# Kernel tuning notes

Measured on AMD Instinct MI355X. Metric: run time of the kernel, lower is better.

Reference implementation:

```python
import jax, jax.numpy as jnp
import numpy as np

B, E, C, M, H = 4, 8, 512, 1024, 4096

def setup_inputs() -> dict:
    key = jax.random.key(0)
    k1, k2, k3, k4, k5 = jax.random.split(key, 5)
    s = 1.0 / np.sqrt(M)
    return {
        "x": jax.random.normal(k1, (B, E, C, M), dtype=jnp.float32),
        "fc1_weight": jax.random.normal(k2, (E, H, M), dtype=jnp.float32) * s,
        "fc1_bias": jax.random.normal(k3, (E, 1, H), dtype=jnp.float32) * 0.02,
        "fc2_weight": jax.random.normal(k4, (E, H, M), dtype=jnp.float32) * (1.0 / np.sqrt(H)),
        "fc2_bias": jax.random.normal(k5, (E, 1, M), dtype=jnp.float32) * 0.02,
    }

def reference(x, fc1_weight, fc1_bias, fc2_weight, fc2_bias):
    # x: [B, E, C, M] -> [E, B*C, M]
    b, e, c, m = x.shape
    xe = jnp.transpose(x, (1, 0, 2, 3)).reshape(e, b * c, m)
    # fc1: [E,T,M] @ [E,M,H] (fp32 grouped GEMM with bias)
    h = jnp.einsum('etm,ehm->eth', xe.astype(jnp.float32), fc1_weight.astype(jnp.float32)) + fc1_bias.astype(jnp.float32)
    h = jax.nn.relu(h)
    # fc2: [E,T,H] @ [E,H,M] + bias (dropout is identity)
    o = jnp.einsum('eth,ehm->etm', h, fc2_weight) + fc2_bias
    o = o.reshape(e, b, c, m)
    return jnp.transpose(o, (1, 0, 2, 3))
```

## Files before the change

### kernel.cpp

```cpp
#include <hip/hip_runtime.h>
#include <hip/hip_bf16.h>

typedef __bf16 bf16x8 __attribute__((ext_vector_type(8)));
typedef float  f32x4  __attribute__((ext_vector_type(4)));

constexpr int Ee = 8, Cc = 512, Mm = 1024, Hh = 4096, Tt = 2048;

__device__ __forceinline__ void async16(void* lds, const void* g) {
  __builtin_amdgcn_global_load_lds(
      (const __attribute__((address_space(1))) void*)g,
      (__attribute__((address_space(3))) void*)lds, 16, 0, 0);
}

#define FENCE() asm volatile("" ::: "memory")
#define BARRIER() do { FENCE(); __builtin_amdgcn_s_barrier(); FENCE(); } while (0)

__device__ __forceinline__ int xcd_swz(int id, int n) {
  const int q = n >> 3, r = n & 7;
  const int x = id & 7, k = id >> 3;
  return (x < r ? x * (q + 1) : r * (q + 1) + (x - r) * q) + k;
}

__device__ __forceinline__ void gemm256(
    const __bf16* __restrict__ aT, const __bf16* __restrict__ bT, const int K,
    __bf16 (*Ab)[2][128][64], __bf16 (*Bb)[2][128][64],
    f32x4 (&acc)[8][4]) {
  const int tid = threadIdx.x;
  const int lane = tid & 63, wid = tid >> 6;
  const int wr = wid >> 2, wcn = wid & 3;
  const int l8 = lane >> 3;
  const int colSwzE = (((lane & 7) ^ l8) << 3);
  const int NT = K >> 6;

  int pblk[2];
  pblk[0] = (lane >> 4) ^ (lane & 7);
  pblk[1] = (4 + (lane >> 4)) ^ (lane & 7);

  bf16x8 aF[8][2];
  bf16x8 bF[2][2];

  auto STAGE = [&](int s, int u) {
    if (s >= NT) return;
    const int d = s & 1;
    if (u < 2) {
      const __bf16* src = aT + (size_t)(u * 128 + wid * 16 + l8) * K + s * 64 + colSwzE;
#pragma unroll
      for (int i = 0; i < 2; ++i)
        async16(&Ab[d][u][wid * 16 + i * 8][0], src + (size_t)(i * 8) * K);
    } else {
      const __bf16* src = bT + (size_t)((u - 2) * 128 + wid * 16 + l8) * K + s * 64 + colSwzE;
#pragma unroll
      for (int i = 0; i < 2; ++i)
        async16(&Bb[d][u - 2][wid * 16 + i * 8][0], src + (size_t)(i * 8) * K);
    }
  };

  STAGE(0, 0); STAGE(0, 1); STAGE(0, 2); STAGE(0, 3);
  STAGE(1, 0); STAGE(1, 1);
  asm volatile("s_waitcnt vmcnt(4)" ::: "memory");
  BARRIER();

  for (int t = 0; t < NT; ++t) {
    const int d = t & 1;
    const char* pa = (const char*)&Ab[d][wr][0][0];
    const char* pb = (const char*)&Bb[d][wcn >> 1][0][0];
    const int brow = (wcn & 1) * 64;

#pragma unroll
    for (int mi = 0; mi < 4; ++mi)
#pragma unroll
      for (int kh = 0; kh < 2; ++kh)
        aF[mi][kh] = *(const bf16x8*)(pa + (mi * 16 + (lane & 15)) * 128 + pblk[kh] * 16);
#pragma unroll
    for (int ni = 0; ni < 2; ++ni)
#pragma unroll
      for (int kh = 0; kh < 2; ++kh)
        bF[ni][kh] = *(const bf16x8*)(pb + (brow + ni * 16 + (lane & 15)) * 128 + pblk[kh] * 16);
    STAGE(t + 1, 2);
    BARRIER();
    __builtin_amdgcn_s_setprio(1);
#pragma unroll
    for (int mi = 0; mi < 4; ++mi)
#pragma unroll
      for (int ni = 0; ni < 2; ++ni)
#pragma unroll
        for (int kh = 0; kh < 2; ++kh)
          acc[mi][ni] = __builtin_amdgcn_mfma_f32_16x16x32_bf16(aF[mi][kh], bF[ni][kh], acc[mi][ni], 0, 0, 0);
    __builtin_amdgcn_s_setprio(0);
    BARRIER();

#pragma unroll
    for (int mi = 0; mi < 4; ++mi)
#pragma unroll
      for (int kh = 0; kh < 2; ++kh)
        aF[4 + mi][kh] = *(const bf16x8*)(pa + ((4 + mi) * 16 + (lane & 15)) * 128 + pblk[kh] * 16);
#pragma unroll
    for (int ni = 0; ni < 2; ++ni)
#pragma unroll
      for (int kh = 0; kh < 2; ++kh)
        bF[ni][kh] = *(const bf16x8*)(pb + (brow + (2 + ni) * 16 + (lane & 15)) * 128 + pblk[kh] * 16);
    STAGE(t + 1, 3);
    BARRIER();
    __builtin_amdgcn_s_setprio(1);
#pragma unroll
    for (int mi = 0; mi < 4; ++mi)
#pragma unroll
      for (int ni = 0; ni < 2; ++ni)
#pragma unroll
        for (int kh = 0; kh < 2; ++kh)
          acc[4 + mi][2 + ni] = __builtin_amdgcn_mfma_f32_16x16x32_bf16(aF[4 + mi][kh], bF[ni][kh], acc[4 + mi][2 + ni], 0, 0, 0);
    __builtin_amdgcn_s_setprio(0);
    BARRIER();

#pragma unroll
    for (int ni = 0; ni < 2; ++ni)
#pragma unroll
      for (int kh = 0; kh < 2; ++kh)
        bF[ni][kh] = *(const bf16x8*)(pb + (brow + (2 + ni) * 16 + (lane & 15)) * 128 + pblk[kh] * 16);
    STAGE(t + 2, 0);
    BARRIER();
    __builtin_amdgcn_s_setprio(1);
#pragma unroll
    for (int mi = 0; mi < 4; ++mi)
#pragma unroll
      for (int ni = 0; ni < 2; ++ni)
#pragma unroll
        for (int kh = 0; kh < 2; ++kh)
          acc[mi][2 + ni] = __builtin_amdgcn_mfma_f32_16x16x32_bf16(aF[mi][kh], bF[ni][kh], acc[mi][2 + ni], 0, 0, 0);
    __builtin_amdgcn_s_setprio(0);
    BARRIER();

#pragma unroll
    for (int ni = 0; ni < 2; ++ni)
#pragma unroll
      for (int kh = 0; kh < 2; ++kh)
        bF[ni][kh] = *(const bf16x8*)(pb + (brow + ni * 16 + (lane & 15)) * 128 + pblk[kh] * 16);
    STAGE(t + 2, 1);
    if (t < NT - 2) { asm volatile("s_waitcnt vmcnt(4)" ::: "memory"); }
    else            { asm volatile("s_waitcnt vmcnt(0)" ::: "memory"); }
    BARRIER();
    __builtin_amdgcn_s_setprio(1);
#pragma unroll
    for (int mi = 0; mi < 4; ++mi)
#pragma unroll
      for (int ni = 0; ni < 2; ++ni)
#pragma unroll
        for (int kh = 0; kh < 2; ++kh)
          acc[4 + mi][ni] = __builtin_amdgcn_mfma_f32_16x16x32_bf16(aF[4 + mi][kh], bF[ni][kh], acc[4 + mi][ni], 0, 0, 0);
    __builtin_amdgcn_s_setprio(0);
    BARRIER();
  }
}

__global__ __launch_bounds__(512, 2) void fc1g_kernel(
    const __bf16* __restrict__ xb, int eOffA,
    const __bf16* __restrict__ w1b, int eOffB,
    const float* __restrict__ b1, __bf16* __restrict__ hb,
    int e0, int t_base, int tcap, int nbT) {
  __shared__ __bf16 Ab[2][2][128][64];
  __shared__ __bf16 Bb[2][2][128][64];
  const int nbN = Hh / 256;
  const int id = xcd_swz(blockIdx.x, gridDim.x);
  const int z = id / (nbN * nbT);
  const int rm = id % (nbN * nbT);
  const int tblk = (rm / nbN) * 256, nblk = (rm % nbN) * 256;
  const int lane = threadIdx.x & 63, wid = threadIdx.x >> 6;
  const int wr = wid >> 2, wcn = wid & 3;

  const __bf16* aT = xb + ((size_t)(eOffA + z) * Tt + t_base + tblk) * Mm;
  const __bf16* bT = w1b + ((size_t)(eOffB + z) * Hh + nblk) * Mm;

  f32x4 acc[8][4];
#pragma unroll
  for (int i = 0; i < 8; ++i)
#pragma unroll
    for (int j = 0; j < 4; ++j) acc[i][j] = (f32x4){0.f, 0.f, 0.f, 0.f};

  gemm256(aT, bT, Mm, Ab, Bb, acc);

  const float* bias = b1 + (size_t)(e0 + z) * Hh;
  const int row0 = tblk + wr * 128 + ((lane >> 4) << 2);
  const int col0 = nblk + wcn * 64 + (lane & 15);
#pragma unroll
  for (int ni = 0; ni < 4; ++ni) {
    const int col = col0 + ni * 16;
    const float bv = bias[col];
#pragma unroll
    for (int mi = 0; mi < 8; ++mi) {
      const int r0 = row0 + mi * 16;
      f32x4 v = acc[mi][ni];
#pragma unroll
      for (int rr = 0; rr < 4; ++rr) {
        float o = v[rr] + bv;
        o = o > 0.f ? o : 0.f;
        hb[((size_t)z * tcap + r0 + rr) * Hh + col] = (__bf16)o;
      }
    }
  }
}

__global__ __launch_bounds__(512, 2) void fc2g_kernel(
    const __bf16* __restrict__ hb, int tcap,
    const __bf16* __restrict__ w2t, int eOffB,
    const float* __restrict__ b2, float* __restrict__ out,
    int e0, int t_base, int nbT) {
  __shared__ __bf16 Ab[2][2][128][64];
  __shared__ __bf16 Bb[2][2][128][64];
  const int nbN = Mm / 256;
  const int id = xcd_swz(blockIdx.x, gridDim.x);
  const int z = id / (nbN * nbT);
  const int rm = id % (nbN * nbT);
  const int tblk = (rm / nbN) * 256, nblk = (rm % nbN) * 256;
  const int lane = threadIdx.x & 63, wid = threadIdx.x >> 6;
  const int wr = wid >> 2, wcn = wid & 3;
  const int e = e0 + z;

  const __bf16* aT = hb + ((size_t)z * tcap + tblk) * Hh;
  const __bf16* bT = w2t + ((size_t)(eOffB + z) * Mm + nblk) * Hh;

  f32x4 acc[8][4];
#pragma unroll
  for (int i = 0; i < 8; ++i)
#pragma unroll
    for (int j = 0; j < 4; ++j) acc[i][j] = (f32x4){0.f, 0.f, 0.f, 0.f};

  gemm256(aT, bT, Hh, Ab, Bb, acc);

  const float* bias = b2 + (size_t)e * Mm;
  const int row0 = tblk + wr * 128 + ((lane >> 4) << 2);
  const int col0 = nblk + wcn * 64 + (lane & 15);
#pragma unroll
  for (int ni = 0; ni < 4; ++ni) {
    const int col = col0 + ni * 16;
    const float bv = bias[col];
#pragma unroll
    for (int mi = 0; mi < 8; ++mi) {
      const int r0 = row0 + mi * 16;
      f32x4 v = acc[mi][ni];
#pragma unroll
      for (int rr = 0; rr < 4; ++rr) {
        const int t = t_base + r0 + rr;
        const int bb = t >> 9, cc = t & 511;
        out[((((size_t)bb * Ee + e) * Cc + cc) << 10) + col] = v[rr] + bv;
      }
    }
  }
}

__global__ __launch_bounds__(256) void cvt_x_kernel(
    const float* __restrict__ x, __bf16* __restrict__ xb, int e0) {
  size_t idx8 = (size_t)blockIdx.x * 256 + threadIdx.x;
  int m8 = (int)(idx8 & 127);
  int t = (int)((idx8 >> 7) & 2047);
  int z = (int)(idx8 >> 18);
  int b = t >> 9, c = t & 511, e = e0 + z;
  const float* src = x + ((((size_t)b * Ee + e) * Cc + c) << 10) + (m8 << 3);
  f32x4 v0 = *(const f32x4*)src;
  f32x4 v1 = *(const f32x4*)(src + 4);
  bf16x8 o;
  o[0] = (__bf16)v0[0]; o[1] = (__bf16)v0[1]; o[2] = (__bf16)v0[2]; o[3] = (__bf16)v0[3];
  o[4] = (__bf16)v1[0]; o[5] = (__bf16)v1[1]; o[6] = (__bf16)v1[2]; o[7] = (__bf16)v1[3];
  *(bf16x8*)(xb + (idx8 << 3)) = o;
}

__global__ __launch_bounds__(256) void cvt_lin_kernel(
    const float* __restrict__ in, __bf16* __restrict__ outb) {
  size_t i8 = (size_t)blockIdx.x * 256 + threadIdx.x;
  const float* src = in + (i8 << 3);
  f32x4 v0 = *(const f32x4*)src;
  f32x4 v1 = *(const f32x4*)(src + 4);
  bf16x8 o;
  o[0] = (__bf16)v0[0]; o[1] = (__bf16)v0[1]; o[2] = (__bf16)v0[2]; o[3] = (__bf16)v0[3];
  o[4] = (__bf16)v1[0]; o[5] = (__bf16)v1[1]; o[6] = (__bf16)v1[2]; o[7] = (__bf16)v1[3];
  *(bf16x8*)(outb + (i8 << 3)) = o;
}

__global__ __launch_bounds__(256) void tr_w2_kernel(
    const float* __restrict__ w2, __bf16* __restrict__ w2t, int e0) {
  __shared__ __bf16 tile[64][68];
  const int z = blockIdx.z, e = e0 + z;
  const int m0 = blockIdx.x * 64, h0 = blockIdx.y * 64;
  const int tid = threadIdx.x;
  const int cg = tid & 15, rg = tid >> 4;
#pragma unroll
  for (int p = 0; p < 4; ++p) {
    int hl = rg + p * 16;
    f32x4 v = *(const f32x4*)(w2 + (((size_t)e * Hh + h0 + hl) << 10) + m0 + (cg << 2));
#pragma unroll
    for (int i = 0; i < 4; ++i) tile[(cg << 2) + i][hl] = (__bf16)v[i];
  }
  __syncthreads();
#pragma unroll
  for (int p = 0; p < 4; ++p) {
    int ml = rg + p * 16;
    uint2 pk = *(const uint2*)(&tile[ml][cg << 2]);
    *(uint2*)(w2t + ((size_t)z * Mm + m0 + ml) * Hh + h0 + (cg << 2)) = pk;
  }
}

extern "C" void kernel_launch(void* const* d_in, const int* in_sizes, int n_in,
                              void* d_out, int out_size, void* d_ws, size_t ws_size,
                              hipStream_t stream) {
  const float* x  = (const float*)d_in[0];
  const float* w1 = (const float*)d_in[1];
  const float* b1 = (const float*)d_in[2];
  const float* w2 = (const float*)d_in[3];
  const float* b2 = (const float*)d_in[4];
  float* out = (float*)d_out;

  const size_t xbS = (size_t)Tt * Mm * 2;
  const size_t w1S = (size_t)Hh * Mm * 2;
  const size_t w2S = (size_t)Mm * Hh * 2;
  const size_t hbS = (size_t)Tt * Hh * 2;
  char* ws = (char*)d_ws;

  if (ws_size >= Ee * (xbS + w1S + w2S + hbS)) {
    __bf16* xb  = (__bf16*)ws;
    __bf16* w1b = (__bf16*)(ws + Ee * xbS);
    __bf16* w2t = (__bf16*)(ws + Ee * (xbS + w1S));
    __bf16* hb  = (__bf16*)(ws + Ee * (xbS + w1S + w2S));
    cvt_x_kernel<<<Ee * 1024, 256, 0, stream>>>(x, xb, 0);
    cvt_lin_kernel<<<Ee * 2048, 256, 0, stream>>>(w1, w1b);
    tr_w2_kernel<<<dim3(Mm / 64, Hh / 64, Ee), 256, 0, stream>>>(w2, w2t, 0);
    fc1g_kernel<<<(Hh / 256) * (Tt / 256) * Ee, 512, 0, stream>>>(xb, 0, w1b, 0, b1, hb, 0, 0, Tt, Tt / 256);
    fc2g_kernel<<<(Mm / 256) * (Tt / 256) * Ee, 512, 0, stream>>>(hb, Tt, w2t, 0, b2, out, 0, 0, Tt / 256);
  } else if (ws_size >= Ee * (xbS + w1S + w2S) + hbS) {
    __bf16* xb  = (__bf16*)ws;
    __bf16* w1b = (__bf16*)(ws + Ee * xbS);
    __bf16* w2t = (__bf16*)(ws + Ee * (xbS + w1S));
    __bf16* hb  = (__bf16*)(ws + Ee * (xbS + w1S + w2S));
    int Gh = (int)((ws_size - Ee * (xbS + w1S + w2S)) / hbS);
    if (Gh > Ee) Gh = Ee;
    cvt_x_kernel<<<Ee * 1024, 256, 0, stream>>>(x, xb, 0);
    cvt_lin_kernel<<<Ee * 2048, 256, 0, stream>>>(w1, w1b);
    tr_w2_kernel<<<dim3(Mm / 64, Hh / 64, Ee), 256, 0, stream>>>(w2, w2t, 0);
    for (int e0 = 0; e0 < Ee; e0 += Gh) {
      int g = (Ee - e0) < Gh ? (Ee - e0) : Gh;
      fc1g_kernel<<<(Hh / 256) * (Tt / 256) * g, 512, 0, stream>>>(xb, e0, w1b, e0, b1, hb, e0, 0, Tt, Tt / 256);
      fc2g_kernel<<<(Mm / 256) * (Tt / 256) * g, 512, 0, stream>>>(hb, Tt, w2t, e0, b2, out, e0, 0, Tt / 256);
    }
  } else if (ws_size >= xbS + w1S + w2S + hbS) {
    int G = (int)(ws_size / (xbS + w1S + w2S + hbS));
    if (G > Ee) G = Ee;
    __bf16* xb  = (__bf16*)ws;
    __bf16* w1b = (__bf16*)(ws + (size_t)G * xbS);
    __bf16* w2t = (__bf16*)(ws + (size_t)G * (xbS + w1S));
    __bf16* hb  = (__bf16*)(ws + (size_t)G * (xbS + w1S + w2S));
    for (int e0 = 0; e0 < Ee; e0 += G) {
      int g = (Ee - e0) < G ? (Ee - e0) : G;
      cvt_x_kernel<<<g * 1024, 256, 0, stream>>>(x, xb, e0);
      cvt_lin_kernel<<<g * 2048, 256, 0, stream>>>(w1 + (size_t)e0 * Hh * Mm, w1b);
      tr_w2_kernel<<<dim3(Mm / 64, Hh / 64, g), 256, 0, stream>>>(w2, w2t, e0);
      fc1g_kernel<<<(Hh / 256) * (Tt / 256) * g, 512, 0, stream>>>(xb, 0, w1b, 0, b1, hb, e0, 0, Tt, Tt / 256);
      fc2g_kernel<<<(Mm / 256) * (Tt / 256) * g, 512, 0, stream>>>(hb, Tt, w2t, 0, b2, out, e0, 0, Tt / 256);
    }
  } else {
    __bf16* xb  = (__bf16*)ws;
    __bf16* w1b = (__bf16*)(ws + xbS);
    __bf16* w2t = (__bf16*)(ws + xbS + w1S);
    __bf16* hb  = (__bf16*)(ws + xbS + w1S + w2S);
    size_t rem = ws_size > (xbS + w1S + w2S) ? ws_size - (xbS + w1S + w2S) : 0;
    int Tc = (int)(rem / ((size_t)Hh * 2)) & ~255;
    if (Tc > Tt) Tc = Tt;
    if (Tc < 256) Tc = 256;
    for (int e0 = 0; e0 < Ee; ++e0) {
      cvt_x_kernel<<<1024, 256, 0, stream>>>(x, xb, e0);
      cvt_lin_kernel<<<2048, 256, 0, stream>>>(w1 + (size_t)e0 * Hh * Mm, w1b);
      tr_w2_kernel<<<dim3(Mm / 64, Hh / 64, 1), 256, 0, stream>>>(w2, w2t, e0);
      for (int t0 = 0; t0 < Tt; t0 += Tc) {
        int tc = (Tt - t0) < Tc ? (Tt - t0) : Tc;
        fc1g_kernel<<<(Hh / 256) * (tc / 256), 512, 0, stream>>>(xb, 0, w1b, 0, b1, hb, e0, t0, Tc, tc / 256);
        fc2g_kernel<<<(Mm / 256) * (tc / 256), 512, 0, stream>>>(hb, Tc, w2t, 0, b2, out, e0, t0, tc / 256);
      }
    }
  }
}
```

Before: 459.1 us.

## Collapse four-phase GEMM loop into two-phase schedule and vectorize epilogue stores

Restructures the main GEMM loop from four barrier-separated MFMA phases into one phase that loads all eight A fragments and issues the next-tile staging up front, with far fewer barriers per K-step. MFMA operands are swapped so the accumulator is transposed, which lets the fc1 and fc2 epilogues write 4 contiguous columns per lane as vector bf16x4/f32x4 stores with a vector bias load instead of scalar strided stores. This cuts barrier overhead and uncoalesced epilogue writes, but raises register pressure from holding 16 A fragments. It also changes the LDS reuse ordering: the STAGE calls for t+1 and t+2 now run before and just after the single barrier, so buffer hazards must still be respected.

```diff
diff --git a/kernel.cpp b/kernel.cpp
--- a/kernel.cpp
+++ b/kernel.cpp
@@ -2,6 +2,7 @@
 #include <hip/hip_bf16.h>
 
 typedef __bf16 bf16x8 __attribute__((ext_vector_type(8)));
+typedef __bf16 bf16x4 __attribute__((ext_vector_type(4)));
 typedef float  f32x4  __attribute__((ext_vector_type(4)));
 
 constexpr int Ee = 8, Cc = 512, Mm = 1024, Hh = 4096, Tt = 2048;
@@ -66,8 +67,10 @@
     const char* pb = (const char*)&Bb[d][wcn >> 1][0][0];
     const int brow = (wcn & 1) * 64;
 
-#pragma unroll
-    for (int mi = 0; mi < 4; ++mi)
+    STAGE(t + 1, 2); STAGE(t + 1, 3);
+
+#pragma unroll
+    for (int mi = 0; mi < 8; ++mi)
 #pragma unroll
       for (int kh = 0; kh < 2; ++kh)
         aF[mi][kh] = *(const bf16x8*)(pa + (mi * 16 + (lane & 15)) * 128 + pblk[kh] * 16);
@@ -76,78 +79,39 @@
 #pragma unroll
       for (int kh = 0; kh < 2; ++kh)
         bF[ni][kh] = *(const bf16x8*)(pb + (brow + ni * 16 + (lane & 15)) * 128 + pblk[kh] * 16);
-    STAGE(t + 1, 2);
+
     BARRIER();
+
+    STAGE(t + 2, 0); STAGE(t + 2, 1);
+
     __builtin_amdgcn_s_setprio(1);
 #pragma unroll
-    for (int mi = 0; mi < 4; ++mi)
+    for (int mi = 0; mi < 8; ++mi)
 #pragma unroll
       for (int ni = 0; ni < 2; ++ni)
 #pragma unroll
         for (int kh = 0; kh < 2; ++kh)
-          acc[mi][ni] = __builtin_amdgcn_mfma_f32_16x16x32_bf16(aF[mi][kh], bF[ni][kh], acc[mi][ni], 0, 0, 0);
+          acc[mi][ni] = __builtin_amdgcn_mfma_f32_16x16x32_bf16(bF[ni][kh], aF[mi][kh], acc[mi][ni], 0, 0, 0);
     __builtin_amdgcn_s_setprio(0);
-    BARRIER();
-
-#pragma unroll
-    for (int mi = 0; mi < 4; ++mi)
-#pragma unroll
-      for (int kh = 0; kh < 2; ++kh)
-        aF[4 + mi][kh] = *(const bf16x8*)(pa + ((4 + mi) * 16 + (lane & 15)) * 128 + pblk[kh] * 16);
+
 #pragma unroll
     for (int ni = 0; ni < 2; ++ni)
 #pragma unroll
       for (int kh = 0; kh < 2; ++kh)
         bF[ni][kh] = *(const bf16x8*)(pb + (brow + (2 + ni) * 16 + (lane & 15)) * 128 + pblk[kh] * 16);
-    STAGE(t + 1, 3);
-    BARRIER();
+
     __builtin_amdgcn_s_setprio(1);
 #pragma unroll
-    for (int mi = 0; mi < 4; ++mi)
+    for (int mi = 0; mi < 8; ++mi)
 #pragma unroll
       for (int ni = 0; ni < 2; ++ni)
 #pragma unroll
         for (int kh = 0; kh < 2; ++kh)
-          acc[4 + mi][2 + ni] = __builtin_amdgcn_mfma_f32_16x16x32_bf16(aF[4 + mi][kh], bF[ni][kh], acc[4 + mi][2 + ni], 0, 0, 0);
+          acc[mi][2 + ni] = __builtin_amdgcn_mfma_f32_16x16x32_bf16(bF[ni][kh], aF[mi][kh], acc[mi][2 + ni], 0, 0, 0);
     __builtin_amdgcn_s_setprio(0);
-    BARRIER();
-
-#pragma unroll
-    for (int ni = 0; ni < 2; ++ni)
-#pragma unroll
-      for (int kh = 0; kh < 2; ++kh)
-        bF[ni][kh] = *(const bf16x8*)(pb + (brow + (2 + ni) * 16 + (lane & 15)) * 128 + pblk[kh] * 16);
-    STAGE(t + 2, 0);
-    BARRIER();
-    __builtin_amdgcn_s_setprio(1);
-#pragma unroll
-    for (int mi = 0; mi < 4; ++mi)
-#pragma unroll
-      for (int ni = 0; ni < 2; ++ni)
-#pragma unroll
-        for (int kh = 0; kh < 2; ++kh)
-          acc[mi][2 + ni] = __builtin_amdgcn_mfma_f32_16x16x32_bf16(aF[mi][kh], bF[ni][kh], acc[mi][2 + ni], 0, 0, 0);
-    __builtin_amdgcn_s_setprio(0);
-    BARRIER();
-
-#pragma unroll
-    for (int ni = 0; ni < 2; ++ni)
-#pragma unroll
-      for (int kh = 0; kh < 2; ++kh)
-        bF[ni][kh] = *(const bf16x8*)(pb + (brow + ni * 16 + (lane & 15)) * 128 + pblk[kh] * 16);
-    STAGE(t + 2, 1);
+
     if (t < NT - 2) { asm volatile("s_waitcnt vmcnt(4)" ::: "memory"); }
     else            { asm volatile("s_waitcnt vmcnt(0)" ::: "memory"); }
-    BARRIER();
-    __builtin_amdgcn_s_setprio(1);
-#pragma unroll
-    for (int mi = 0; mi < 4; ++mi)
-#pragma unroll
-      for (int ni = 0; ni < 2; ++ni)
-#pragma unroll
-        for (int kh = 0; kh < 2; ++kh)
-          acc[4 + mi][ni] = __builtin_amdgcn_mfma_f32_16x16x32_bf16(aF[4 + mi][kh], bF[ni][kh], acc[4 + mi][ni], 0, 0, 0);
-    __builtin_amdgcn_s_setprio(0);
     BARRIER();
   }
 }
@@ -179,22 +143,21 @@
   gemm256(aT, bT, Mm, Ab, Bb, acc);
 
   const float* bias = b1 + (size_t)(e0 + z) * Hh;
-  const int row0 = tblk + wr * 128 + ((lane >> 4) << 2);
-  const int col0 = nblk + wcn * 64 + (lane & 15);
 #pragma unroll
   for (int ni = 0; ni < 4; ++ni) {
-    const int col = col0 + ni * 16;
-    const float bv = bias[col];
+    const int n0 = nblk + wcn * 64 + ni * 16 + ((lane >> 4) << 2);
+    const f32x4 b4 = *(const f32x4*)(bias + n0);
 #pragma unroll
     for (int mi = 0; mi < 8; ++mi) {
-      const int r0 = row0 + mi * 16;
+      const int trow = tblk + wr * 128 + mi * 16 + (lane & 15);
       f32x4 v = acc[mi][ni];
+      bf16x4 o;
 #pragma unroll
       for (int rr = 0; rr < 4; ++rr) {
-        float o = v[rr] + bv;
-        o = o > 0.f ? o : 0.f;
-        hb[((size_t)z * tcap + r0 + rr) * Hh + col] = (__bf16)o;
+        float f = v[rr] + b4[rr];
+        o[rr] = (__bf16)(f > 0.f ? f : 0.f);
       }
+      *(bf16x4*)(hb + ((size_t)z * tcap + trow) * Hh + n0) = o;
     }
   }
 }
@@ -227,22 +190,18 @@
   gemm256(aT, bT, Hh, Ab, Bb, acc);
 
   const float* bias = b2 + (size_t)e * Mm;
-  const int row0 = tblk + wr * 128 + ((lane >> 4) << 2);
-  const int col0 = nblk + wcn * 64 + (lane & 15);
 #pragma unroll
   for (int ni = 0; ni < 4; ++ni) {
-    const int col = col0 + ni * 16;
-    const float bv = bias[col];
+    const int m0 = nblk + wcn * 64 + ni * 16 + ((lane >> 4) << 2);
+    const f32x4 b4 = *(const f32x4*)(bias + m0);
 #pragma unroll
     for (int mi = 0; mi < 8; ++mi) {
-      const int r0 = row0 + mi * 16;
+      const int t = t_base + tblk + wr * 128 + mi * 16 + (lane & 15);
+      const int bb = t >> 9, cc = t & 511;
       f32x4 v = acc[mi][ni];
 #pragma unroll
-      for (int rr = 0; rr < 4; ++rr) {
-        const int t = t_base + r0 + rr;
-        const int bb = t >> 9, cc = t & 511;
-        out[((((size_t)bb * Ee + e) * Cc + cc) << 10) + col] = v[rr] + bv;
-      }
+      for (int rr = 0; rr < 4; ++rr) v[rr] += b4[rr];
+      *(f32x4*)(out + ((((size_t)bb * Ee + e) * Cc + cc) << 10) + m0) = v;
     }
   }
 }
```

Result: faster. 426.8 us (-7.0%).
